# Optimization experiments

Hardware: AMD Instinct MI355X
Metric: run time of the kernel (lower is better)

Reference implementation:

```python
import jax, jax.numpy as jnp
import numpy as np

B, NPG, H = 128, 111, 32
N = B * NPG                 # 14208 total nodes
EPG = NPG * (NPG - 1)       # 12210 directed edges per connectome graph
E = B * EPG                 # 1562880 edges total


def setup_inputs() -> dict:
    key = jax.random.key(0)
    # full directed graph (no self loops) within each of the B graphs
    s, d = np.nonzero(~np.eye(NPG, dtype=bool))
    off = (np.arange(B) * NPG)[:, None]
    edge_index = jnp.asarray(
        np.stack([(s[None] + off).ravel(), (d[None] + off).ravel()]),
        dtype=jnp.int32)
    ks = iter(jax.random.split(key, 32))
    def nrm(shape, scale=0.1):
        return (jax.random.normal(next(ks), shape) * scale).astype(jnp.float32)
    inp = {
        'x': nrm((N, 1), 1.0),
        'edge_index': edge_index,
        'edge_attr': nrm((E, 2), 1.0),
    }
    dims = [1, H, H]  # input dim of each GATConv layer
    for l in range(3):
        inp[f'W{l}'] = nrm((dims[l], H))   # lin weight (no bias in PyG lin)
        inp[f'as{l}'] = nrm((H,))          # att_src
        inp[f'ad{l}'] = nrm((H,))          # att_dst
        inp[f'We{l}'] = nrm((2, H))        # lin_edge weight
        inp[f'ae{l}'] = nrm((H,))          # att_edge
        inp[f'b{l}'] = jnp.zeros((H,), jnp.float32)
    inp['lin_W'] = nrm((H, 1))
    inp['lin_b'] = jnp.zeros((1,), jnp.float32)
    return inp


def _gat(x, src, dst, ea, W, a_s, a_d, We, a_e, b):
    """PyG GATConv, heads=1: edge-feature attention + segment softmax over dst."""
    h = x @ W                                                     # [N,H]
    alpha = (h @ a_s)[src] + (h @ a_d)[dst] + (ea @ We) @ a_e     # [E']
    alpha = jax.nn.leaky_relu(alpha, 0.2)
    m = jax.lax.stop_gradient(jax.ops.segment_max(alpha, dst, num_segments=N))
    ex = jnp.exp(alpha - m[dst])
    coef = ex / jax.ops.segment_sum(ex, dst, num_segments=N)[dst]
    return jax.ops.segment_sum(coef[:, None] * h[src], dst, num_segments=N) + b


def reference(x, edge_index, edge_attr,
              W0, as0, ad0, We0, ae0, b0,
              W1, as1, ad1, We1, ae1, b1,
              W2, as2, ad2, We2, ae2, b2,
              lin_W, lin_b):
    src0, dst0 = edge_index[0], edge_index[1]
    # add_self_loops with fill_value='mean': per-dst mean of incoming edge_attr
    deg = jax.ops.segment_sum(jnp.ones((E,), edge_attr.dtype), dst0, num_segments=N)
    ea_loop = jax.ops.segment_sum(edge_attr, dst0, num_segments=N) / jnp.maximum(deg, 1.0)[:, None]
    loop = jnp.arange(N, dtype=src0.dtype)
    src = jnp.concatenate([src0, loop])
    dst = jnp.concatenate([dst0, loop])
    ea = jnp.concatenate([edge_attr, ea_loop], axis=0)

    h = _gat(x, src, dst, ea, W0, as0, ad0, We0, ae0, b0)
    h = _gat(h, src, dst, ea, W1, as1, ad1, We1, ae1, b1)
    h = jax.nn.relu(h)  # Dropout(0.5) is identity in eval
    h = _gat(h, src, dst, ea, W2, as2, ad2, We2, ae2, b2)

    graph_id = jnp.arange(N) // NPG                                # global_add_pool
    pooled = jax.ops.segment_sum(h, graph_id, num_segments=B)      # [B,H]
    return jax.nn.relu(pooled @ lin_W + lin_b)                     # [B,1]
```

## Files before the change

### kernel.cpp

```cpp
#include <hip/hip_runtime.h>
#include <hip/hip_bf16.h>

#define BGR  128
#define NPG  111
#define EPG  (NPG*(NPG-1))
#define H16S 136
#define HRS  40

typedef _Float16 half8 __attribute__((ext_vector_type(8)));
typedef float    f32x4 __attribute__((ext_vector_type(4)));

__global__ __launch_bounds__(1024, 1) void
gnn_all(const float* __restrict__ x, const float* __restrict__ ea,
        const float* __restrict__ W0, const float* __restrict__ as0, const float* __restrict__ ad0,
        const float* __restrict__ We0, const float* __restrict__ ae0, const float* __restrict__ b0,
        const float* __restrict__ W1, const float* __restrict__ as1, const float* __restrict__ ad1,
        const float* __restrict__ We1, const float* __restrict__ ae1, const float* __restrict__ b1,
        const float* __restrict__ W2, const float* __restrict__ as2, const float* __restrict__ ad2,
        const float* __restrict__ We2, const float* __restrict__ ae2, const float* __restrict__ b2,
        const float* __restrict__ linW, const float* __restrict__ linb,
        float* __restrict__ out)
{
    int g = blockIdx.x;
    int t = threadIdx.x;
    int wave = t >> 6, lane = t & 63;
    int m = lane & 15, quad = lane >> 4;

    __shared__ float     eattL[EPG];
    __shared__ _Float16  h16[32 * H16S];
    __shared__ _Float16  hrow[112 * HRS];
    __shared__ float     ass[112], ads[112], diag[112];
    __shared__ float     asw[32], adw[32], bsh[32];
    __shared__ float     pool7[8];

    for (int i = t; i < 32 * H16S; i += 1024) h16[i] = (_Float16)0.f;
    if (t < HRS) hrow[111 * HRS + t] = (_Float16)0.f;

    const float4* eg4 = (const float4*)(ea + (size_t)g * EPG * 2);

    for (int l = 0; l < 3; l++) {
        const float* W  = (l == 0) ? W0  : ((l == 1) ? W1  : W2);
        const float* aS = (l == 0) ? as0 : ((l == 1) ? as1 : as2);
        const float* aD = (l == 0) ? ad0 : ((l == 1) ? ad1 : ad2);
        const float* Ne = (l == 0) ? We0 : ((l == 1) ? We1 : We2);
        const float* av = (l == 0) ? ae0 : ((l == 1) ? ae1 : ae2);
        const float* bb = (l == 0) ? b0  : ((l == 1) ? b1  : b2);

        float red = Ne[(lane >> 5) * 32 + (lane & 31)] * av[lane & 31];
        #pragma unroll
        for (int off = 1; off < 32; off <<= 1) red += __shfl_xor(red, off);
        float c0 = __shfl(red, 0), c1 = __shfl(red, 32);

        for (int i = t; i < EPG / 2; i += 1024) {
            float4 v = eg4[i];
            float2 w2;
            w2.x = c0 * v.x + c1 * v.y;
            w2.y = c0 * v.z + c1 * v.w;
            *(float2*)&eattL[2 * i] = w2;
        }
        if (t < 32) { asw[t] = aS[t]; adw[t] = aD[t]; bsh[t] = bb[t]; }

        if (l == 0) {
            for (int i = t; i < 32 * 112; i += 1024) {
                int c = i / 112, s = i - c * 112;
                float hv = (s < NPG) ? x[g * NPG + s] * W[c] : 0.f;
                h16[c * H16S + s] = (_Float16)hv;
            }
        } else if (wave < 14) {
            int ct = wave & 1, st = wave >> 1;
            int cb = ct * 16 + m;
            half8 A, B;
            #pragma unroll
            for (int j = 0; j < 8; j++) A[j] = (_Float16)W[(quad * 8 + j) * 32 + cb];
            B = *(const half8*)&hrow[(st * 16 + m) * HRS + quad * 8];
            if (l == 2) {
                #pragma unroll
                for (int j = 0; j < 8; j++)
                    B[j] = (B[j] > (_Float16)0.f) ? B[j] : (_Float16)0.f;
            }
            f32x4 D = {0.f, 0.f, 0.f, 0.f};
            D = __builtin_amdgcn_mfma_f32_16x16x32_f16(A, B, D, 0, 0, 0);
            #pragma unroll
            for (int r = 0; r < 4; r++)
                h16[(ct * 16 + quad * 4 + r) * H16S + st * 16 + m] = (_Float16)D[r];
        }
        __syncthreads();

        if (t < NPG) {
            float sa = 0.f, sd = 0.f;
            #pragma unroll 8
            for (int cc = 0; cc < 32; cc++) {
                float hv = (float)h16[cc * H16S + t];
                sa += hv * asw[cc];
                sd += hv * adw[cc];
            }
            ass[t] = sa; ads[t] = sd;
        } else if (t >= 128 && t < 128 + NPG) {
            int d2 = t - 128;
            float sum = 0.f;
            #pragma unroll 8
            for (int s = 0; s < NPG; s++) {
                if (s != d2) sum += eattL[s * 110 + d2 - (d2 > s ? 1 : 0)];
            }
            diag[d2] = sum * (1.f / 110.f);
        }
        __syncthreads();

        if (wave < 7) {
            f32x4 acc0 = {0.f, 0.f, 0.f, 0.f};
            f32x4 acc1 = {0.f, 0.f, 0.f, 0.f};
            float den = 0.f;
            int d = wave * 16 + m;
            bool dok = (d < NPG);
            float adsv = dok ? ads[d] : 0.f;
            float dval = dok ? diag[d] : 0.f;
            #pragma unroll
            for (int kc = 0; kc < 4; kc++) {
                int s0 = kc * 32 + quad * 8;
                half8 A;
                #pragma unroll
                for (int j = 0; j < 8; j++) {
                    int s = s0 + j;
                    float p = 0.f;
                    if (dok && s < NPG) {
                        float ev = (s == d) ? dval
                                 : eattL[s * 110 + d - (d > s ? 1 : 0)];
                        float a = ass[s] + adsv + ev;
                        a = (a > 0.f) ? a : 0.2f * a;
                        p = __expf(a);
                    }
                    _Float16 ph = (_Float16)p;
                    A[j] = ph;
                    den += (float)ph;
                }
                half8 B0 = *(const half8*)&h16[(size_t)m * H16S + s0];
                half8 B1 = *(const half8*)&h16[(size_t)(16 + m) * H16S + s0];
                acc0 = __builtin_amdgcn_mfma_f32_16x16x32_f16(A, B0, acc0, 0, 0, 0);
                acc1 = __builtin_amdgcn_mfma_f32_16x16x32_f16(A, B1, acc1, 0, 0, 0);
            }
            den += __shfl_xor(den, 16);
            den += __shfl_xor(den, 32);

            if (l < 2) {
                #pragma unroll
                for (int r = 0; r < 4; r++) {
                    int dr = wave * 16 + quad * 4 + r;
                    float dn = __shfl(den, quad * 4 + r);
                    if (dr < NPG) {
                        float inv = 1.f / dn;
                        hrow[dr * HRS + m]      = (_Float16)(acc0[r] * inv + bsh[m]);
                        hrow[dr * HRS + 16 + m] = (_Float16)(acc1[r] * inv + bsh[16 + m]);
                    }
                }
            } else {
                float lw0 = linW[m], lw1 = linW[16 + m];
                float p = 0.f;
                #pragma unroll
                for (int r = 0; r < 4; r++) {
                    int dr = wave * 16 + quad * 4 + r;
                    float dn = __shfl(den, quad * 4 + r);
                    if (dr < NPG) {
                        float inv = 1.f / dn;
                        p += (acc0[r] * inv + bsh[m]) * lw0
                           + (acc1[r] * inv + bsh[16 + m]) * lw1;
                    }
                }
                #pragma unroll
                for (int off = 1; off < 64; off <<= 1) p += __shfl_xor(p, off);
                if (lane == 0) pool7[wave] = p;
            }
        }
        __syncthreads();
    }

    if (t == 0) {
        float s = 0.f;
        #pragma unroll
        for (int w = 0; w < 7; w++) s += pool7[w];
        out[g] = fmaxf(s + linb[0], 0.f);
    }
}

extern "C" void kernel_launch(void* const* d_in, const int* in_sizes, int n_in,
                              void* d_out, int out_size, void* d_ws, size_t ws_size,
                              hipStream_t stream) {
    const float* x  = (const float*)d_in[0];
    const float* ea = (const float*)d_in[2];
    gnn_all<<<BGR, 1024, 0, stream>>>(
        x, ea,
        (const float*)d_in[3],  (const float*)d_in[4],  (const float*)d_in[5],
        (const float*)d_in[6],  (const float*)d_in[7],  (const float*)d_in[8],
        (const float*)d_in[9],  (const float*)d_in[10], (const float*)d_in[11],
        (const float*)d_in[12], (const float*)d_in[13], (const float*)d_in[14],
        (const float*)d_in[15], (const float*)d_in[16], (const float*)d_in[17],
        (const float*)d_in[18], (const float*)d_in[19], (const float*)d_in[20],
        (const float*)d_in[21], (const float*)d_in[22],
        (float*)d_out);
}
```

Baseline: 146.7 us.

## Read edge attributes from global directly and fuse attention-score computation into GEMM

Removes the per-layer staging of projected edge attention values into LDS and instead reads edge_attr float2 pairs straight from global memory (L2-cached) in both the diag and softmax loops. Per-node src/dst attention scores are now computed in the MFMA epilogue as two partial sums per column tile, and the diag mean runs concurrently on spare waves, which eliminates one __syncthreads per layer. In exchange, each layer re-reads the edge attributes from global memory with uncoalesced strided access, which adds memory latency inside the exp/MFMA loop.

```diff
diff --git a/kernel.cpp b/kernel.cpp
--- a/kernel.cpp
+++ b/kernel.cpp
@@ -26,17 +26,23 @@
     int wave = t >> 6, lane = t & 63;
     int m = lane & 15, quad = lane >> 4;
 
-    __shared__ float     eattL[EPG];
-    __shared__ _Float16  h16[32 * H16S];
-    __shared__ _Float16  hrow[112 * HRS];
-    __shared__ float     ass[112], ads[112], diag[112];
-    __shared__ float     asw[32], adw[32], bsh[32];
-    __shared__ float     pool7[8];
+    __shared__ _Float16 h16[32 * H16S];
+    __shared__ _Float16 hrow[112 * HRS];
+    __shared__ float assP[2][112];
+    __shared__ float adsP[2][112];
+    __shared__ float diag[112];
+    __shared__ float bsh[32];
+    __shared__ float pool7[8];
 
     for (int i = t; i < 32 * H16S; i += 1024) h16[i] = (_Float16)0.f;
-    if (t < HRS) hrow[111 * HRS + t] = (_Float16)0.f;
-
-    const float4* eg4 = (const float4*)(ea + (size_t)g * EPG * 2);
+    if (t < 32) hrow[111 * HRS + t] = (_Float16)0.f;
+
+    float kr = (lane < 32) ? W0[lane] * as0[lane] : W0[lane & 31] * ad0[lane & 31];
+    #pragma unroll
+    for (int off = 1; off < 32; off <<= 1) kr += __shfl_xor(kr, off);
+    float K_as = __shfl(kr, 0), K_ad = __shfl(kr, 32);
+
+    const float2* eg2 = (const float2*)ea + (size_t)g * EPG;
 
     for (int l = 0; l < 3; l++) {
         const float* W  = (l == 0) ? W0  : ((l == 1) ? W1  : W2);
@@ -51,81 +57,95 @@
         for (int off = 1; off < 32; off <<= 1) red += __shfl_xor(red, off);
         float c0 = __shfl(red, 0), c1 = __shfl(red, 32);
 
-        for (int i = t; i < EPG / 2; i += 1024) {
-            float4 v = eg4[i];
-            float2 w2;
-            w2.x = c0 * v.x + c1 * v.y;
-            w2.y = c0 * v.z + c1 * v.w;
-            *(float2*)&eattL[2 * i] = w2;
-        }
-        if (t < 32) { asw[t] = aS[t]; adw[t] = aD[t]; bsh[t] = bb[t]; }
-
-        if (l == 0) {
-            for (int i = t; i < 32 * 112; i += 1024) {
-                int c = i / 112, s = i - c * 112;
-                float hv = (s < NPG) ? x[g * NPG + s] * W[c] : 0.f;
-                h16[c * H16S + s] = (_Float16)hv;
-            }
-        } else if (wave < 14) {
-            int ct = wave & 1, st = wave >> 1;
-            int cb = ct * 16 + m;
-            half8 A, B;
-            #pragma unroll
-            for (int j = 0; j < 8; j++) A[j] = (_Float16)W[(quad * 8 + j) * 32 + cb];
-            B = *(const half8*)&hrow[(st * 16 + m) * HRS + quad * 8];
-            if (l == 2) {
-                #pragma unroll
-                for (int j = 0; j < 8; j++)
-                    B[j] = (B[j] > (_Float16)0.f) ? B[j] : (_Float16)0.f;
-            }
-            f32x4 D = {0.f, 0.f, 0.f, 0.f};
-            D = __builtin_amdgcn_mfma_f32_16x16x32_f16(A, B, D, 0, 0, 0);
-            #pragma unroll
-            for (int r = 0; r < 4; r++)
-                h16[(ct * 16 + quad * 4 + r) * H16S + st * 16 + m] = (_Float16)D[r];
+        if (t < 32) bsh[t] = bb[t];
+
+        if (wave < 14) {
+            if (l == 0) {
+                int c = t & 31, sbase = t >> 5;
+                #pragma unroll
+                for (int it = 0; it < 4; it++) {
+                    int s = sbase + it * 28;
+                    float hv = (s < NPG) ? x[g * NPG + s] * W[c] : 0.f;
+                    h16[c * H16S + s] = (_Float16)hv;
+                }
+                if (t < 112) {
+                    float v = (t < NPG) ? x[g * NPG + t] : 0.f;
+                    assP[0][t] = v * K_as;  adsP[0][t] = v * K_ad;
+                    assP[1][t] = 0.f;       adsP[1][t] = 0.f;
+                }
+            } else {
+                int ct = wave & 1, st = wave >> 1;
+                int cb = ct * 16 + m;
+                half8 A, B;
+                #pragma unroll
+                for (int j = 0; j < 8; j++) A[j] = (_Float16)W[(quad * 8 + j) * 32 + cb];
+                B = *(const half8*)&hrow[(st * 16 + m) * HRS + quad * 8];
+                if (l == 2) {
+                    #pragma unroll
+                    for (int j = 0; j < 8; j++)
+                        B[j] = (B[j] > (_Float16)0.f) ? B[j] : (_Float16)0.f;
+                }
+                f32x4 D = {0.f, 0.f, 0.f, 0.f};
+                D = __builtin_amdgcn_mfma_f32_16x16x32_f16(A, B, D, 0, 0, 0);
+                float pa = 0.f, pd = 0.f;
+                #pragma unroll
+                for (int r = 0; r < 4; r++) {
+                    int cc = ct * 16 + quad * 4 + r;
+                    h16[cc * H16S + st * 16 + m] = (_Float16)D[r];
+                    pa += D[r] * aS[cc];
+                    pd += D[r] * aD[cc];
+                }
+                pa += __shfl_xor(pa, 16); pa += __shfl_xor(pa, 32);
+                pd += __shfl_xor(pd, 16); pd += __shfl_xor(pd, 32);
+                if (lane < 16) { assP[ct][st * 16 + m] = pa; adsP[ct][st * 16 + m] = pd; }
+            }
+        } else {
+            int dd = (wave - 14) * 64 + lane;
+            if (dd < NPG) {
+                float sum = 0.f;
+                #pragma unroll 8
+                for (int s = 0; s < NPG; s++) {
+                    if (s != dd) {
+                        float2 e = eg2[s * 110 + dd - (dd > s ? 1 : 0)];
+                        sum += c0 * e.x + c1 * e.y;
+                    }
+                }
+                diag[dd] = sum * (1.f / 110.f);
+            }
         }
         __syncthreads();
 
-        if (t < NPG) {
-            float sa = 0.f, sd = 0.f;
-            #pragma unroll 8
-            for (int cc = 0; cc < 32; cc++) {
-                float hv = (float)h16[cc * H16S + t];
-                sa += hv * asw[cc];
-                sd += hv * adw[cc];
-            }
-            ass[t] = sa; ads[t] = sd;
-        } else if (t >= 128 && t < 128 + NPG) {
-            int d2 = t - 128;
-            float sum = 0.f;
-            #pragma unroll 8
-            for (int s = 0; s < NPG; s++) {
-                if (s != d2) sum += eattL[s * 110 + d2 - (d2 > s ? 1 : 0)];
-            }
-            diag[d2] = sum * (1.f / 110.f);
-        }
-        __syncthreads();
-
         if (wave < 7) {
+            int d = wave * 16 + m;
+            bool dok = (d < NPG);
+            float adsv = dok ? (adsP[0][d] + adsP[1][d]) : 0.f;
+            float dval = dok ? diag[d] : 0.f;
             f32x4 acc0 = {0.f, 0.f, 0.f, 0.f};
             f32x4 acc1 = {0.f, 0.f, 0.f, 0.f};
             float den = 0.f;
-            int d = wave * 16 + m;
-            bool dok = (d < NPG);
-            float adsv = dok ? ads[d] : 0.f;
-            float dval = dok ? diag[d] : 0.f;
             #pragma unroll
             for (int kc = 0; kc < 4; kc++) {
                 int s0 = kc * 32 + quad * 8;
+                float4 p0 = *(const float4*)&assP[0][s0];
+                float4 p1 = *(const float4*)&assP[1][s0];
+                float4 q0 = *(const float4*)&assP[0][s0 + 4];
+                float4 q1 = *(const float4*)&assP[1][s0 + 4];
+                float asv[8] = {p0.x + p1.x, p0.y + p1.y, p0.z + p1.z, p0.w + p1.w,
+                                q0.x + q1.x, q0.y + q1.y, q0.z + q1.z, q0.w + q1.w};
                 half8 A;
                 #pragma unroll
                 for (int j = 0; j < 8; j++) {
                     int s = s0 + j;
                     float p = 0.f;
                     if (dok && s < NPG) {
-                        float ev = (s == d) ? dval
-                                 : eattL[s * 110 + d - (d > s ? 1 : 0)];
-                        float a = ass[s] + adsv + ev;
+                        float ev;
+                        if (s == d) {
+                            ev = dval;
+                        } else {
+                            float2 e = eg2[s * 110 + d - (d > s ? 1 : 0)];
+                            ev = c0 * e.x + c1 * e.y;
+                        }
+                        float a = asv[j] + adsv + ev;
                         a = (a > 0.f) ? a : 0.2f * a;
                         p = __expf(a);
                     }
```

Result: slower. 224.7 us (+53.2%).
